# Kernel optimization log

Hardware: AMD Instinct MI355X
Metric: run time of the kernel (lower is better)

Reference implementation:

```python
import jax, jax.numpy as jnp
import numpy as np

B, N, D, H = 4, 2048, 256, 4
DH = D // H
SS = DH ** -0.25  # sqrt(scale), applied to both qk0 and qk1
EPS = 1e-5


def _split_heads(t):
    # [B, N, D] -> [B, H, N, DH]
    b, n, _ = t.shape
    return t.reshape(b, n, H, DH).transpose(0, 2, 1, 3)


def _merge_heads(t):
    # [B, H, N, DH] -> [B, N, D]
    b, h, n, dh = t.shape
    return t.transpose(0, 2, 1, 3).reshape(b, n, h * dh)


def _layernorm(x, g, b):
    mu = jnp.mean(x, axis=-1, keepdims=True)
    var = jnp.mean(jnp.square(x - mu), axis=-1, keepdims=True)
    return (x - mu) * jax.lax.rsqrt(var + EPS) * g + b


def setup_inputs() -> dict:
    key = jax.random.key(0)
    ks = jax.random.split(key, 16)
    s = 0.02
    return {
        "x0": jax.random.normal(ks[0], (B, N, D), jnp.float32),
        "x1": jax.random.normal(ks[1], (B, N, D), jnp.float32),
        # weights stored as [in, out] (y = x @ W + b), matching torch Linear math
        "Wqk": jax.random.normal(ks[2], (D, D), jnp.float32) * s,
        "bqk": jnp.zeros((D,), jnp.float32),
        "Wv": jax.random.normal(ks[3], (D, D), jnp.float32) * s,
        "bv": jnp.zeros((D,), jnp.float32),
        "Wo": jax.random.normal(ks[4], (D, D), jnp.float32) * s,
        "bo": jnp.zeros((D,), jnp.float32),
        "W1": jax.random.normal(ks[5], (2 * D, 2 * D), jnp.float32) * s,
        "b1": jnp.zeros((2 * D,), jnp.float32),
        "ln_g": jnp.ones((2 * D,), jnp.float32),
        "ln_b": jnp.zeros((2 * D,), jnp.float32),
        "W2": jax.random.normal(ks[6], (2 * D, D), jnp.float32) * s,
        "b2": jnp.zeros((D,), jnp.float32),
    }


def reference(x0, x1, Wqk, bqk, Wv, bv, Wo, bo, W1, b1, ln_g, ln_b, W2, b2):
    qk0 = _split_heads(x0 @ Wqk + bqk) * SS  # [B,H,N,DH]
    qk1 = _split_heads(x1 @ Wqk + bqk) * SS
    v0 = _split_heads(x0 @ Wv + bv)
    v1 = _split_heads(x1 @ Wv + bv)

    # single shared similarity matrix, reused for both softmax directions
    sim = jnp.einsum("bhid,bhjd->bhij", qk0, qk1)  # [B,H,N0,N1]
    attn01 = jax.nn.softmax(sim, axis=-1)                      # rows over j
    attn10 = jax.nn.softmax(jnp.swapaxes(sim, -1, -2), axis=-1)  # rows over i

    m0 = jnp.einsum("bhij,bhjd->bhid", attn01, v1)  # [B,H,N0,DH]
    m1 = jnp.einsum("bhji,bhjd->bhid", jnp.swapaxes(attn10, -1, -2), v0)

    m0 = _merge_heads(m0) @ Wo + bo  # [B,N,D]
    m1 = _merge_heads(m1) @ Wo + bo

    def ffn(x, m):
        h = jnp.concatenate([x, m], axis=-1) @ W1 + b1
        h = jax.nn.gelu(_layernorm(h, ln_g, ln_b), approximate=False)
        return x + h @ W2 + b2

    return ffn(x0, m0), ffn(x1, m1)
```

## Files before the change

### kernel.cpp

```cpp
#include <hip/hip_runtime.h>
#include <hip/hip_bf16.h>
#include <math.h>

#define DEV static __device__ __forceinline__

typedef float f32x4 __attribute__((ext_vector_type(4)));
typedef short s16x8 __attribute__((ext_vector_type(8)));
typedef unsigned short u16;
typedef unsigned int u32;
typedef u32 u32x2 __attribute__((ext_vector_type(2)));
typedef u16 u16x4 __attribute__((ext_vector_type(4)));

#define ROWS 16384
#define SSCALE 0.35355339059327379f

DEV f32x4 mfma16(s16x8 a, s16x8 b, f32x4 c) {
  return __builtin_amdgcn_mfma_f32_16x16x32_bf16(a, b, c, 0, 0, 0);
}

DEV float bf2f(u16 x) { u32 u = ((u32)x) << 16; float f; __builtin_memcpy(&f, &u, 4); return f; }
DEV u16 f2bf(float x) { __hip_bfloat16 b = __float2bfloat16(x); u16 r; __builtin_memcpy(&r, &b, 2); return r; }

DEV void gload_lds16(const void* g, void* l) {
  __builtin_amdgcn_global_load_lds((const __attribute__((address_space(1))) u32*)g,
                                   (__attribute__((address_space(3))) u32*)l, 16, 0, 0);
}

__global__ __launch_bounds__(256) void k_prep(
    const float* __restrict__ x0, const float* __restrict__ x1,
    const float* __restrict__ Wqk, const float* __restrict__ Wv,
    const float* __restrict__ Wo, const float* __restrict__ W1,
    const float* __restrict__ W2,
    u16* __restrict__ bt_qkv, u16* __restrict__ bt_o,
    u16* __restrict__ bt_1, u16* __restrict__ bt_2, u16* __restrict__ Xb)
{
  int tid = blockIdx.x * 256 + threadIdx.x;
  if (tid < 131072) {
    int c = tid >> 8, k = tid & 255;
    float v = (c < 256) ? Wqk[k * 256 + c] : Wv[k * 256 + (c - 256)];
    bt_qkv[tid] = f2bf(v);
  } else if (tid < 131072 + 65536) {
    int t = tid - 131072; int c = t >> 8, k = t & 255;
    bt_o[t] = f2bf(Wo[k * 256 + c]);
  } else if (tid < 131072 + 65536 + 262144) {
    int t = tid - (131072 + 65536); int c = t >> 9, k = t & 511;
    bt_1[t] = f2bf(W1[k * 512 + c]);
  } else if (tid < 589824) {
    int t = tid - (131072 + 65536 + 262144); int c = t >> 9, k = t & 511;
    bt_2[t] = f2bf(W2[k * 256 + c]);
  } else {
    int t = tid - 589824;
    float v = (t < 8192 * 256) ? x0[t] : x1[t - 8192 * 256];
    Xb[t] = f2bf(v);
  }
}

template <int KD, int K1, int EPI, int BN>
__global__ __launch_bounds__(256, 2) void k_gemm(
    const u16* __restrict__ A1, const u16* __restrict__ A2,
    const u16* __restrict__ Bt,
    const float* __restrict__ bias, const float* __restrict__ bias2,
    const float* __restrict__ res0, const float* __restrict__ res1,
    u16* __restrict__ outb, u16* __restrict__ outb2,
    float* __restrict__ outf, int Ncols)
{
  constexpr int MR = (BN == 128) ? 4 : 2;
  __shared__ char lds[16384 + 2 * BN * 64];
  char* ldsA = lds;
  char* ldsB = lds + 16384;
  const int tid = threadIdx.x;
  const int lane = tid & 63;
  const int w = tid >> 6;
  const int wm = (BN == 128) ? (w >> 1) : w;
  const int wn = (BN == 128) ? (w & 1) : 0;
  const int g = lane >> 4, li = lane & 15;
  const int m0 = blockIdx.x * 128, n0 = blockIdx.y * BN;

  auto stage = [&](int buf, int t) {
    const int k0 = t * 32;
#pragma unroll
    for (int it = 0; it < 2; ++it) {
      int chunk = it * 256 + w * 64 + lane;
      int row = chunk >> 2, c = chunk & 3;
      int kc = k0 + ((c ^ ((row >> 1) & 3)) << 3);
      const u16* src = (kc < K1) ? (A1 + (size_t)(m0 + row) * K1 + kc)
                                 : (A2 + (size_t)(m0 + row) * (KD - K1) + (kc - K1));
      gload_lds16(src, ldsA + buf * 8192 + (it * 256 + w * 64) * 16);
    }
#pragma unroll
    for (int it = 0; it < BN / 64; ++it) {
      int chunk = it * 256 + w * 64 + lane;
      int row = chunk >> 2, c = chunk & 3;
      int kc = k0 + ((c ^ ((row >> 1) & 3)) << 3);
      gload_lds16(Bt + (size_t)(n0 + row) * KD + kc,
                  ldsB + buf * (BN * 64) + (it * 256 + w * 64) * 16);
    }
  };

  f32x4 acc[MR][4] = {};

  stage(0, 0);
  __syncthreads();
  const int NT = KD / 32;
  for (int t = 0; t < NT; ++t) {
    if (t + 1 < NT) stage((t + 1) & 1, t + 1);
    const char* bufA = ldsA + (t & 1) * 8192;
    const char* bufB = ldsB + (t & 1) * (BN * 64);
    s16x8 af[MR], bfr[4];
#pragma unroll
    for (int rt = 0; rt < MR; ++rt) {
      int row = wm * (MR * 16) + rt * 16 + li;
      af[rt] = *(const s16x8*)(bufA + row * 64 + ((g ^ ((row >> 1) & 3)) << 4));
    }
#pragma unroll
    for (int ct = 0; ct < 4; ++ct) {
      int col = wn * 64 + ct * 16 + li;
      bfr[ct] = *(const s16x8*)(bufB + col * 64 + ((g ^ ((col >> 1) & 3)) << 4));
    }
#pragma unroll
    for (int rt = 0; rt < MR; ++rt)
#pragma unroll
      for (int ct = 0; ct < 4; ++ct)
        acc[rt][ct] = mfma16(af[rt], bfr[ct], acc[rt][ct]);
    __syncthreads();
  }

#pragma unroll
  for (int rt = 0; rt < MR; ++rt) {
#pragma unroll
    for (int ct = 0; ct < 4; ++ct) {
      const int growb = m0 + wm * (MR * 16) + rt * 16 + g * 4;
      const int gcol = n0 + wn * 64 + ct * 16 + li;
      if (EPI == 0) {
        const int dir = growb >> 13, b = (growb >> 11) & 3, n = growb & 2047;
        if (gcol < 256) {
          const int h = gcol >> 6, dh = gcol & 63;
#pragma unroll
          for (int r = 0; r < 4; ++r) {
            float q = (acc[rt][ct][r] + bias[gcol]) * SSCALE;
            outb[((size_t)(dir * 16 + b * 4 + h) * 2048 + (n + r)) * 64 + dh] = f2bf(q);
          }
        } else {
          const int c2 = gcol - 256, h = c2 >> 6, dh = c2 & 63;
          u16x4 pk;
#pragma unroll
          for (int r = 0; r < 4; ++r) pk[r] = f2bf(acc[rt][ct][r] + bias2[c2]);
          *(u16x4*)(outb2 + ((size_t)(dir * 16 + b * 4 + h) * 64 + dh) * 2048 + n) = pk;
        }
      } else if (EPI == 1) {
#pragma unroll
        for (int r = 0; r < 4; ++r)
          outb[(size_t)(growb + r) * Ncols + gcol] = f2bf(acc[rt][ct][r] + bias[gcol]);
      } else {
#pragma unroll
        for (int r = 0; r < 4; ++r) {
          int grow = growb + r;
          float x = (grow < 8192) ? res0[(size_t)grow * 256 + gcol]
                                  : res1[(size_t)(grow - 8192) * 256 + gcol];
          outf[(size_t)grow * 256 + gcol] = acc[rt][ct][r] + bias[gcol] + x;
        }
      }
    }
  }
}

__global__ __launch_bounds__(256, 3) void k_attn(
    const u16* __restrict__ qk, const u16* __restrict__ vt,
    float* __restrict__ Opart, float* __restrict__ lpart)
{
  __shared__ char Kl[2][8192];
  __shared__ char Vl[2][8192];
  __shared__ char Pl[4][4096];
  const int tid = threadIdx.x, lane = tid & 63, w = tid >> 6;
  const int g = lane >> 4, li = lane & 15;
  const int qblk = blockIdx.x & 15;
  const int half = (blockIdx.x >> 4) & 1;
  const int p = blockIdx.x >> 5;
  const int dir = p & 1;
  const int bh = p >> 1;
  const int pidx = dir * 16 + bh;
  const char* Qg = (const char*)qk + (size_t)pidx * 2048 * 128;
  const char* Kg = (const char*)qk + (size_t)((dir ^ 1) * 16 + bh) * 2048 * 128;
  const char* Vg = (const char*)vt + (size_t)((dir ^ 1) * 16 + bh) * 2048 * 128;
  const int q0 = qblk * 128 + w * 32;

  s16x8 qf[2][2];
#pragma unroll
  for (int qt = 0; qt < 2; ++qt)
#pragma unroll
    for (int ks = 0; ks < 2; ++ks)
      qf[qt][ks] = *(const s16x8*)(Qg + (size_t)(q0 + qt * 16 + li) * 128 + ks * 64 + g * 16);

  auto stageKV = [&](int buf, int jt) {
    const size_t krow0 = (size_t)(half * 1024 + jt * 64);
#pragma unroll
    for (int it = 0; it < 2; ++it) {
      int chunk = it * 256 + w * 64 + lane;
      int row = chunk >> 3, c = chunk & 7;
      int cc = (c ^ (row & 7)) << 4;
      gload_lds16(Kg + (krow0 + row) * 128 + cc, &Kl[buf][(it * 256 + w * 64) * 16]);
    }
#pragma unroll
    for (int it = 0; it < 2; ++it) {
      int chunk = it * 256 + w * 64 + lane;
      int row = chunk >> 3, c = chunk & 7;
      int cc = (c ^ (row & 7)) << 4;
      gload_lds16(Vg + (size_t)row * 4096 + half * 2048 + jt * 128 + cc,
                  &Vl[buf][(it * 256 + w * 64) * 16]);
    }
  };

  f32x4 acco[2][4] = {};
  float accl[2] = {0.f, 0.f};

  stageKV(0, 0);
  __syncthreads();
  for (int jt = 0; jt < 16; ++jt) {
    if (jt + 1 < 16) stageKV((jt + 1) & 1, jt + 1);
    const char* Kb = Kl[jt & 1];
    const char* Vb = Vl[jt & 1];

#pragma unroll
    for (int kt = 0; kt < 4; ++kt) {
      const int krow = kt * 16 + li;
      s16x8 kf0 = *(const s16x8*)(Kb + krow * 128 + ((g ^ (krow & 7)) << 4));
      s16x8 kf1 = *(const s16x8*)(Kb + krow * 128 + (((4 + g) ^ (krow & 7)) << 4));
#pragma unroll
      for (int qt = 0; qt < 2; ++qt) {
        f32x4 s = {0.f, 0.f, 0.f, 0.f};
        s = mfma16(kf0, qf[qt][0], s);
        s = mfma16(kf1, qf[qt][1], s);
        float p0 = __expf(s[0]), p1 = __expf(s[1]);
        float p2 = __expf(s[2]), p3 = __expf(s[3]);
        accl[qt] += (p0 + p1) + (p2 + p3);
        u32x2 pk;
        pk.x = (u32)f2bf(p0) | ((u32)f2bf(p1) << 16);
        pk.y = (u32)f2bf(p2) | ((u32)f2bf(p3) << 16);
        int addr = ((qt * 16 + li) * 128 + kt * 32 + g * 8) ^ ((li & 7) << 4);
        *(u32x2*)(&Pl[w][addr]) = pk;
      }
    }

#pragma unroll
    for (int ks = 0; ks < 2; ++ks) {
      s16x8 vfr[4];
#pragma unroll
      for (int dt = 0; dt < 4; ++dt) {
        const int vrow = dt * 16 + li;
        vfr[dt] = *(const s16x8*)(Vb + vrow * 128 + (((ks * 4 + g) ^ (vrow & 7)) << 4));
      }
#pragma unroll
      for (int qt = 0; qt < 2; ++qt) {
        s16x8 pf = *(const s16x8*)(
            &Pl[w][((qt * 16 + li) * 128 + ks * 64 + g * 16) ^ ((li & 7) << 4)]);
#pragma unroll
        for (int dt = 0; dt < 4; ++dt)
          acco[qt][dt] = mfma16(pf, vfr[dt], acco[qt][dt]);
      }
    }
    __syncthreads();
  }

#pragma unroll
  for (int qt = 0; qt < 2; ++qt) {
    float v = accl[qt];
    v += __shfl_xor(v, 16);
    v += __shfl_xor(v, 32);
    accl[qt] = v;
  }

  const int b = bh >> 2, h = bh & 3;
  const size_t rowbase = (size_t)dir * 8192 + (size_t)b * 2048 + q0;
  float* Oh = Opart + (size_t)half * 4194304;
#pragma unroll
  for (int qt = 0; qt < 2; ++qt)
#pragma unroll
    for (int dt = 0; dt < 4; ++dt)
#pragma unroll
      for (int r = 0; r < 4; ++r)
        Oh[(rowbase + qt * 16 + g * 4 + r) * 256 + h * 64 + dt * 16 + li] = acco[qt][dt][r];
  if (lane < 16) {
#pragma unroll
    for (int qt = 0; qt < 2; ++qt)
      lpart[half * 65536 + pidx * 2048 + q0 + qt * 16 + li] = accl[qt];
  }
}

__global__ __launch_bounds__(256) void k_combine(
    const float* __restrict__ Op, const float* __restrict__ lp,
    u16* __restrict__ m_all)
{
  int t = blockIdx.x * 256 + threadIdx.x;
  int row = t >> 6, quad = t & 63;
  int dh0 = quad * 4;
  int dir = row >> 13, b = (row >> 11) & 3, n = row & 2047, h = dh0 >> 6;
  int pidx = dir * 16 + b * 4 + h;
  float l = lp[pidx * 2048 + n] + lp[65536 + pidx * 2048 + n];
  float invl = 1.0f / l;
  f32x4 o0 = *(const f32x4*)(Op + (size_t)row * 256 + dh0);
  f32x4 o1 = *(const f32x4*)(Op + 4194304 + (size_t)row * 256 + dh0);
  u16x4 r4;
#pragma unroll
  for (int j = 0; j < 4; ++j) r4[j] = f2bf((o0[j] + o1[j]) * invl);
  *(u16x4*)(m_all + (size_t)row * 256 + dh0) = r4;
}

__global__ __launch_bounds__(256) void k_ln_gelu(
    const u16* __restrict__ h, const float* __restrict__ lg,
    const float* __restrict__ lb, u16* __restrict__ o)
{
  int lane = threadIdx.x & 63;
  size_t row = blockIdx.x * 4 + (threadIdx.x >> 6);
  s16x8 v = *(const s16x8*)(h + row * 512 + lane * 8);
  float f[8], s = 0.f, s2 = 0.f;
#pragma unroll
  for (int j = 0; j < 8; ++j) { f[j] = bf2f((u16)v[j]); s += f[j]; s2 += f[j] * f[j]; }
#pragma unroll
  for (int m = 1; m < 64; m <<= 1) { s += __shfl_xor(s, m); s2 += __shfl_xor(s2, m); }
  float mu = s * (1.0f / 512.0f);
  float var = s2 * (1.0f / 512.0f) - mu * mu;
  float rs = rsqrtf(var + 1e-5f);
  s16x8 ov;
#pragma unroll
  for (int j = 0; j < 8; ++j) {
    int c = lane * 8 + j;
    float y = (f[j] - mu) * rs * lg[c] + lb[c];
    float ge = 0.5f * y * (1.0f + erff(y * 0.70710678118654752f));
    ov[j] = (short)f2bf(ge);
  }
  *(s16x8*)(o + row * 512 + lane * 8) = ov;
}

extern "C" void kernel_launch(void* const* d_in, const int* in_sizes, int n_in,
                              void* d_out, int out_size, void* d_ws, size_t ws_size,
                              hipStream_t stream)
{
  const float* x0  = (const float*)d_in[0];
  const float* x1  = (const float*)d_in[1];
  const float* Wqk = (const float*)d_in[2];
  const float* bqk = (const float*)d_in[3];
  const float* Wv  = (const float*)d_in[4];
  const float* bv  = (const float*)d_in[5];
  const float* Wo  = (const float*)d_in[6];
  const float* bo  = (const float*)d_in[7];
  const float* W1  = (const float*)d_in[8];
  const float* b1  = (const float*)d_in[9];
  const float* lg  = (const float*)d_in[10];
  const float* lb  = (const float*)d_in[11];
  const float* W2  = (const float*)d_in[12];
  const float* b2  = (const float*)d_in[13];
  float* out = (float*)d_out;
  char* ws = (char*)d_ws;

  u16*   Xb    = (u16*)(ws + 0);
  u16*   qk    = (u16*)(ws + 8388608);
  u16*   vt    = (u16*)(ws + 16777216);
  u16*   m_all = (u16*)(ws + 25165824);
  float* lpart = (float*)(ws + 33554432);
  u16*   mo    = (u16*)(ws + 34078720);
  float* Opart = (float*)(ws + 42467328);
  u16*   hpre  = (u16*)(ws + 42467328);
  u16*   gact  = (u16*)(ws + 59244544);
  u16*   btqkv = (u16*)(ws + 76021760);
  u16*   bto   = (u16*)(ws + 76283904);
  u16*   bt1   = (u16*)(ws + 76414976);
  u16*   bt2   = (u16*)(ws + 76939264);

  k_prep<<<dim3(18688), dim3(256), 0, stream>>>(x0, x1, Wqk, Wv, Wo, W1, W2,
                                                btqkv, bto, bt1, bt2, Xb);
  k_gemm<256, 256, 0, 128><<<dim3(128, 4), dim3(256), 0, stream>>>(
      Xb, nullptr, btqkv, bqk, bv, nullptr, nullptr, qk, vt, nullptr, 512);
  k_attn<<<dim3(1024), dim3(256), 0, stream>>>(qk, vt, Opart, lpart);
  k_combine<<<dim3(4096), dim3(256), 0, stream>>>(Opart, lpart, m_all);
  k_gemm<256, 256, 1, 64><<<dim3(128, 4), dim3(256), 0, stream>>>(
      m_all, nullptr, bto, bo, nullptr, nullptr, nullptr, mo, nullptr, nullptr, 256);
  k_gemm<512, 256, 1, 128><<<dim3(128, 4), dim3(256), 0, stream>>>(
      Xb, mo, bt1, b1, nullptr, nullptr, nullptr, hpre, nullptr, nullptr, 512);
  k_ln_gelu<<<dim3(4096), dim3(256), 0, stream>>>(hpre, lg, lb, gact);
  k_gemm<512, 512, 3, 64><<<dim3(128, 4), dim3(256), 0, stream>>>(
      gact, nullptr, bt2, b2, nullptr, x0, x1, nullptr, nullptr, out, 256);
}
```

Before: 235.7 us.

## Fold Wo into W1, drop split-KV attention and combine, vectorize prep

Folds the output projection algebraically into the first FFN weight: computes Wo·W1[256:] and a folded bias in the prep kernel, which removes the Wo GEMM and its intermediate buffer. The attention kernel no longer splits KV into halves. Each block now processes 64 query rows over all 2048 keys and normalizes in-kernel, so the fp32 partial outputs and the combine kernel go away. Prep is rewritten with vectorized conversion and LDS-tiled weight transposes, and the attention grid uses a swizzled block order. The trade-offs are a serial 256-length dot product per folded weight element in prep, less per-block Q reuse in attention, and an extra bf16 rounding of the folded weights.

```diff
diff --git a/kernel.cpp b/kernel.cpp
--- a/kernel.cpp
+++ b/kernel.cpp
@@ -10,8 +10,8 @@
 typedef unsigned int u32;
 typedef u32 u32x2 __attribute__((ext_vector_type(2)));
 typedef u16 u16x4 __attribute__((ext_vector_type(4)));
-
-#define ROWS 16384
+typedef u16 u16x8 __attribute__((ext_vector_type(8)));
+
 #define SSCALE 0.35355339059327379f
 
 DEV f32x4 mfma16(s16x8 a, s16x8 b, f32x4 c) {
@@ -30,28 +30,67 @@
     const float* __restrict__ x0, const float* __restrict__ x1,
     const float* __restrict__ Wqk, const float* __restrict__ Wv,
     const float* __restrict__ Wo, const float* __restrict__ W1,
-    const float* __restrict__ W2,
-    u16* __restrict__ bt_qkv, u16* __restrict__ bt_o,
-    u16* __restrict__ bt_1, u16* __restrict__ bt_2, u16* __restrict__ Xb)
-{
-  int tid = blockIdx.x * 256 + threadIdx.x;
-  if (tid < 131072) {
-    int c = tid >> 8, k = tid & 255;
-    float v = (c < 256) ? Wqk[k * 256 + c] : Wv[k * 256 + (c - 256)];
-    bt_qkv[tid] = f2bf(v);
-  } else if (tid < 131072 + 65536) {
-    int t = tid - 131072; int c = t >> 8, k = t & 255;
-    bt_o[t] = f2bf(Wo[k * 256 + c]);
-  } else if (tid < 131072 + 65536 + 262144) {
-    int t = tid - (131072 + 65536); int c = t >> 9, k = t & 511;
-    bt_1[t] = f2bf(W1[k * 512 + c]);
-  } else if (tid < 589824) {
-    int t = tid - (131072 + 65536 + 262144); int c = t >> 9, k = t & 511;
-    bt_2[t] = f2bf(W2[k * 256 + c]);
+    const float* __restrict__ W2, const float* __restrict__ bo,
+    const float* __restrict__ b1,
+    u16* __restrict__ btqkv, u16* __restrict__ btF,
+    u16* __restrict__ bt2, float* __restrict__ bc, u16* __restrict__ Xb)
+{
+  const int blk = blockIdx.x, tid = threadIdx.x;
+  if (blk < 2048) {
+    int idx = blk * 2048 + tid * 8;
+    const float* src = (idx < 2097152) ? (x0 + idx) : (x1 + (idx - 2097152));
+    f32x4 va = *(const f32x4*)src;
+    f32x4 vb = *(const f32x4*)(src + 4);
+    u16x8 o;
+#pragma unroll
+    for (int j = 0; j < 4; ++j) { o[j] = f2bf(va[j]); o[4 + j] = f2bf(vb[j]); }
+    *(u16x8*)(Xb + idx) = o;
+  } else if (blk < 2144) {
+    __shared__ float T[64][65];
+    int tb = blk - 2048;
+    const float* src; u16* dst; int sld, dld, kr0, c0, drow0;
+    if (tb < 16)      { src = Wqk; dst = btqkv; sld = 256; dld = 256; drow0 = 0;
+                        kr0 = (tb >> 2) * 64; c0 = (tb & 3) * 64; }
+    else if (tb < 32) { tb -= 16; src = Wv; dst = btqkv; sld = 256; dld = 256; drow0 = 256;
+                        kr0 = (tb >> 2) * 64; c0 = (tb & 3) * 64; }
+    else if (tb < 64) { tb -= 32; src = W1; dst = btF; sld = 512; dld = 512; drow0 = 0;
+                        kr0 = (tb >> 3) * 64; c0 = (tb & 7) * 64; }
+    else              { tb -= 64; src = W2; dst = bt2; sld = 256; dld = 512; drow0 = 0;
+                        kr0 = (tb >> 2) * 64; c0 = (tb & 3) * 64; }
+    int r = tid >> 2, cq = (tid & 3) * 16;
+#pragma unroll
+    for (int q = 0; q < 4; ++q) {
+      f32x4 v = *(const f32x4*)(src + (size_t)(kr0 + r) * sld + c0 + cq + q * 4);
+#pragma unroll
+      for (int e = 0; e < 4; ++e) T[r][cq + q * 4 + e] = v[e];
+    }
+    __syncthreads();
+    int c = tid >> 2, kq = (tid & 3) * 16;
+#pragma unroll
+    for (int q = 0; q < 2; ++q) {
+      u16x8 o;
+#pragma unroll
+      for (int e = 0; e < 8; ++e) o[e] = f2bf(T[kq + q * 8 + e][c]);
+      *(u16x8*)(dst + (size_t)(drow0 + c0 + c) * dld + kr0 + kq + q * 8) = o;
+    }
+  } else if (blk < 2656) {
+    int wb = blk - 2144;
+    int i = wb >> 1;
+    int n = (wb & 1) * 256 + tid;
+    float a0 = 0.f, a1 = 0.f, a2 = 0.f, a3 = 0.f;
+    for (int j = 0; j < 256; j += 4) {
+      a0 = fmaf(Wo[i * 256 + j],     W1[(size_t)(256 + j) * 512 + n], a0);
+      a1 = fmaf(Wo[i * 256 + j + 1], W1[(size_t)(257 + j) * 512 + n], a1);
+      a2 = fmaf(Wo[i * 256 + j + 2], W1[(size_t)(258 + j) * 512 + n], a2);
+      a3 = fmaf(Wo[i * 256 + j + 3], W1[(size_t)(259 + j) * 512 + n], a3);
+    }
+    btF[(size_t)n * 512 + 256 + i] = f2bf((a0 + a1) + (a2 + a3));
   } else {
-    int t = tid - 589824;
-    float v = (t < 8192 * 256) ? x0[t] : x1[t - 8192 * 256];
-    Xb[t] = f2bf(v);
+    int n = (blk - 2656) * 256 + tid;
+    float acc = b1[n];
+    for (int j = 0; j < 256; ++j)
+      acc = fmaf(bo[j], W1[(size_t)(256 + j) * 512 + n], acc);
+    bc[n] = acc;
   }
 }
 
@@ -132,20 +171,20 @@
       const int growb = m0 + wm * (MR * 16) + rt * 16 + g * 4;
       const int gcol = n0 + wn * 64 + ct * 16 + li;
       if (EPI == 0) {
-        const int dir = growb >> 13, b = (growb >> 11) & 3, n = growb & 2047;
+        const int dir = growb >> 13, bb = (growb >> 11) & 3, n = growb & 2047;
         if (gcol < 256) {
           const int h = gcol >> 6, dh = gcol & 63;
 #pragma unroll
           for (int r = 0; r < 4; ++r) {
             float q = (acc[rt][ct][r] + bias[gcol]) * SSCALE;
-            outb[((size_t)(dir * 16 + b * 4 + h) * 2048 + (n + r)) * 64 + dh] = f2bf(q);
+            outb[((size_t)(dir * 16 + bb * 4 + h) * 2048 + (n + r)) * 64 + dh] = f2bf(q);
           }
         } else {
           const int c2 = gcol - 256, h = c2 >> 6, dh = c2 & 63;
           u16x4 pk;
 #pragma unroll
           for (int r = 0; r < 4; ++r) pk[r] = f2bf(acc[rt][ct][r] + bias2[c2]);
-          *(u16x4*)(outb2 + ((size_t)(dir * 16 + b * 4 + h) * 64 + dh) * 2048 + n) = pk;
+          *(u16x4*)(outb2 + ((size_t)(dir * 16 + bb * 4 + h) * 64 + dh) * 2048 + n) = pk;
         }
       } else if (EPI == 1) {
 #pragma unroll
@@ -164,145 +203,97 @@
   }
 }
 
-__global__ __launch_bounds__(256, 3) void k_attn(
-    const u16* __restrict__ qk, const u16* __restrict__ vt,
-    float* __restrict__ Opart, float* __restrict__ lpart)
+__global__ __launch_bounds__(256, 4) void k_attn(
+    const u16* __restrict__ qk, const u16* __restrict__ vt, u16* __restrict__ m_all)
 {
   __shared__ char Kl[2][8192];
   __shared__ char Vl[2][8192];
-  __shared__ char Pl[4][4096];
+  __shared__ char Pl[4][2048];
   const int tid = threadIdx.x, lane = tid & 63, w = tid >> 6;
   const int g = lane >> 4, li = lane & 15;
-  const int qblk = blockIdx.x & 15;
-  const int half = (blockIdx.x >> 4) & 1;
-  const int p = blockIdx.x >> 5;
-  const int dir = p & 1;
-  const int bh = p >> 1;
-  const int pidx = dir * 16 + bh;
-  const char* Qg = (const char*)qk + (size_t)pidx * 2048 * 128;
-  const char* Kg = (const char*)qk + (size_t)((dir ^ 1) * 16 + bh) * 2048 * 128;
-  const char* Vg = (const char*)vt + (size_t)((dir ^ 1) * 16 + bh) * 2048 * 128;
-  const int q0 = qblk * 128 + w * 32;
-
-  s16x8 qf[2][2];
-#pragma unroll
-  for (int qt = 0; qt < 2; ++qt)
-#pragma unroll
-    for (int ks = 0; ks < 2; ++ks)
-      qf[qt][ks] = *(const s16x8*)(Qg + (size_t)(q0 + qt * 16 + li) * 128 + ks * 64 + g * 16);
+  const int sw = (blockIdx.x & 7) * 128 + (blockIdx.x >> 3);
+  const int qblk = sw & 31;
+  const int p = sw >> 5;
+  const int dir = p >> 4, bh = p & 15;
+  const char* Qg = (const char*)qk + (size_t)p * 262144;
+  const char* Kg = (const char*)qk + (size_t)((dir ^ 1) * 16 + bh) * 262144;
+  const char* Vg = (const char*)vt + (size_t)((dir ^ 1) * 16 + bh) * 262144;
+  const int q0 = qblk * 64 + w * 16;
+
+  s16x8 qf0 = *(const s16x8*)(Qg + (size_t)(q0 + li) * 128 + g * 16);
+  s16x8 qf1 = *(const s16x8*)(Qg + (size_t)(q0 + li) * 128 + 64 + g * 16);
 
   auto stageKV = [&](int buf, int jt) {
-    const size_t krow0 = (size_t)(half * 1024 + jt * 64);
 #pragma unroll
     for (int it = 0; it < 2; ++it) {
       int chunk = it * 256 + w * 64 + lane;
       int row = chunk >> 3, c = chunk & 7;
       int cc = (c ^ (row & 7)) << 4;
-      gload_lds16(Kg + (krow0 + row) * 128 + cc, &Kl[buf][(it * 256 + w * 64) * 16]);
+      gload_lds16(Kg + (size_t)(jt * 64 + row) * 128 + cc, &Kl[buf][(it * 256 + w * 64) * 16]);
     }
 #pragma unroll
     for (int it = 0; it < 2; ++it) {
       int chunk = it * 256 + w * 64 + lane;
       int row = chunk >> 3, c = chunk & 7;
       int cc = (c ^ (row & 7)) << 4;
-      gload_lds16(Vg + (size_t)row * 4096 + half * 2048 + jt * 128 + cc,
-                  &Vl[buf][(it * 256 + w * 64) * 16]);
+      gload_lds16(Vg + (size_t)row * 4096 + jt * 128 + cc, &Vl[buf][(it * 256 + w * 64) * 16]);
     }
   };
 
-  f32x4 acco[2][4] = {};
-  float accl[2] = {0.f, 0.f};
+  f32x4 acco[4] = {};
+  float accl = 0.f;
 
   stageKV(0, 0);
   __syncthreads();
-  for (int jt = 0; jt < 16; ++jt) {
-    if (jt + 1 < 16) stageKV((jt + 1) & 1, jt + 1);
+  for (int jt = 0; jt < 32; ++jt) {
+    if (jt + 1 < 32) stageKV((jt + 1) & 1, jt + 1);
     const char* Kb = Kl[jt & 1];
     const char* Vb = Vl[jt & 1];
 
 #pragma unroll
     for (int kt = 0; kt < 4; ++kt) {
       const int krow = kt * 16 + li;
-      s16x8 kf0 = *(const s16x8*)(Kb + krow * 128 + ((g ^ (krow & 7)) << 4));
-      s16x8 kf1 = *(const s16x8*)(Kb + krow * 128 + (((4 + g) ^ (krow & 7)) << 4));
-#pragma unroll
-      for (int qt = 0; qt < 2; ++qt) {
-        f32x4 s = {0.f, 0.f, 0.f, 0.f};
-        s = mfma16(kf0, qf[qt][0], s);
-        s = mfma16(kf1, qf[qt][1], s);
-        float p0 = __expf(s[0]), p1 = __expf(s[1]);
-        float p2 = __expf(s[2]), p3 = __expf(s[3]);
-        accl[qt] += (p0 + p1) + (p2 + p3);
-        u32x2 pk;
-        pk.x = (u32)f2bf(p0) | ((u32)f2bf(p1) << 16);
-        pk.y = (u32)f2bf(p2) | ((u32)f2bf(p3) << 16);
-        int addr = ((qt * 16 + li) * 128 + kt * 32 + g * 8) ^ ((li & 7) << 4);
-        *(u32x2*)(&Pl[w][addr]) = pk;
-      }
+      s16x8 kf0 = *(const s16x8*)(Kb + krow * 128 + ((g ^ (li & 7)) << 4));
+      s16x8 kf1 = *(const s16x8*)(Kb + krow * 128 + (((4 + g) ^ (li & 7)) << 4));
+      f32x4 s = {0.f, 0.f, 0.f, 0.f};
+      s = mfma16(kf0, qf0, s);
+      s = mfma16(kf1, qf1, s);
+      float p0 = __expf(s[0]), p1 = __expf(s[1]);
+      float p2 = __expf(s[2]), p3 = __expf(s[3]);
+      accl += (p0 + p1) + (p2 + p3);
+      u32x2 pk;
+      pk.x = (u32)f2bf(p0) | ((u32)f2bf(p1) << 16);
+      pk.y = (u32)f2bf(p2) | ((u32)f2bf(p3) << 16);
+      *(u32x2*)(&Pl[w][(li * 128 + kt * 32 + g * 8) ^ ((li & 7) << 4)]) = pk;
     }
 
 #pragma unroll
     for (int ks = 0; ks < 2; ++ks) {
-      s16x8 vfr[4];
+      s16x8 pf = *(const s16x8*)(&Pl[w][(li * 128 + ks * 64 + g * 16) ^ ((li & 7) << 4)]);
 #pragma unroll
       for (int dt = 0; dt < 4; ++dt) {
         const int vrow = dt * 16 + li;
-        vfr[dt] = *(const s16x8*)(Vb + vrow * 128 + (((ks * 4 + g) ^ (vrow & 7)) << 4));
+        s16x8 vfr = *(const s16x8*)(Vb + vrow * 128 + (((ks * 4 + g) ^ (li & 7)) << 4));
+        acco[dt] = mfma16(pf, vfr, acco[dt]);
       }
-#pragma unroll
-      for (int qt = 0; qt < 2; ++qt) {
-        s16x8 pf = *(const s16x8*)(
-            &Pl[w][((qt * 16 + li) * 128 + ks * 64 + g * 16) ^ ((li & 7) << 4)]);
-#pragma unroll
-        for (int dt = 0; dt < 4; ++dt)
-          acco[qt][dt] = mfma16(pf, vfr[dt], acco[qt][dt]);
-      }
     }
     __syncthreads();
   }
 
-#pragma unroll
-  for (int qt = 0; qt < 2; ++qt) {
-    float v = accl[qt];
-    v += __shfl_xor(v, 16);
-    v += __shfl_xor(v, 32);
-    accl[qt] = v;
-  }
-
-  const int b = bh >> 2, h = bh & 3;
-  const size_t rowbase = (size_t)dir * 8192 + (size_t)b * 2048 + q0;
-  float* Oh = Opart + (size_t)half * 4194304;
-#pragma unroll
-  for (int qt = 0; qt < 2; ++qt)
-#pragma unroll
-    for (int dt = 0; dt < 4; ++dt)
-#pragma unroll
-      for (int r = 0; r < 4; ++r)
-        Oh[(rowbase + qt * 16 + g * 4 + r) * 256 + h * 64 + dt * 16 + li] = acco[qt][dt][r];
-  if (lane < 16) {
-#pragma unroll
-    for (int qt = 0; qt < 2; ++qt)
-      lpart[half * 65536 + pidx * 2048 + q0 + qt * 16 + li] = accl[qt];
-  }
-}
-
-__global__ __launch_bounds__(256) void k_combine(
-    const float* __restrict__ Op, const float* __restrict__ lp,
-    u16* __restrict__ m_all)
-{
-  int t = blockIdx.x * 256 + threadIdx.x;
-  int row = t >> 6, quad = t & 63;
-  int dh0 = quad * 4;
-  int dir = row >> 13, b = (row >> 11) & 3, n = row & 2047, h = dh0 >> 6;
-  int pidx = dir * 16 + b * 4 + h;
-  float l = lp[pidx * 2048 + n] + lp[65536 + pidx * 2048 + n];
-  float invl = 1.0f / l;
-  f32x4 o0 = *(const f32x4*)(Op + (size_t)row * 256 + dh0);
-  f32x4 o1 = *(const f32x4*)(Op + 4194304 + (size_t)row * 256 + dh0);
-  u16x4 r4;
-#pragma unroll
-  for (int j = 0; j < 4; ++j) r4[j] = f2bf((o0[j] + o1[j]) * invl);
-  *(u16x4*)(m_all + (size_t)row * 256 + dh0) = r4;
+  accl += __shfl_xor(accl, 16);
+  accl += __shfl_xor(accl, 32);
+  float inv = 1.0f / accl;
+  float invq[4];
+#pragma unroll
+  for (int r = 0; r < 4; ++r) invq[r] = __shfl(inv, g * 4 + r);
+
+  const int bb = bh >> 2, h = bh & 3;
+  const size_t rowb = (size_t)dir * 8192 + (size_t)bb * 2048 + q0 + g * 4;
+#pragma unroll
+  for (int dt = 0; dt < 4; ++dt)
+#pragma unroll
+    for (int r = 0; r < 4; ++r)
+      m_all[(rowb + r) * 256 + h * 64 + dt * 16 + li] = f2bf(acco[dt][r] * invq[r]);
 }
 
 __global__ __launch_bounds__(256) void k_ln_gelu(
@@ -356,26 +347,20 @@
   u16*   qk    = (u16*)(ws + 8388608);
   u16*   vt    = (u16*)(ws + 16777216);
   u16*   m_all = (u16*)(ws + 25165824);
-  float* lpart = (float*)(ws + 33554432);
-  u16*   mo    = (u16*)(ws + 34078720);
-  float* Opart = (float*)(ws + 42467328);
-  u16*   hpre  = (u16*)(ws + 42467328);
-  u16*   gact  = (u16*)(ws + 59244544);
-  u16*   btqkv = (u16*)(ws + 76021760);
-  u16*   bto   = (u16*)(ws + 76283904);
-  u16*   bt1   = (u16*)(ws + 76414976);
-  u16*   bt2   = (u16*)(ws + 76939264);
-
-  k_prep<<<dim3(18688), dim3(256), 0, stream>>>(x0, x1, Wqk, Wv, Wo, W1, W2,
-                                                btqkv, bto, bt1, bt2, Xb);
+  u16*   hpre  = (u16*)(ws + 33554432);
+  u16*   gact  = (u16*)(ws + 50331648);
+  u16*   btqkv = (u16*)(ws + 67108864);
+  u16*   btF   = (u16*)(ws + 67371008);
+  u16*   bt2   = (u16*)(ws + 67895296);
+  float* bc    = (float*)(ws + 68419584);
+
+  k_prep<<<dim3(2658), dim3(256), 0, stream>>>(x0, x1, Wqk, Wv, Wo, W1, W2, bo, b1,
+                                               btqkv, btF, bt2, bc, Xb);
   k_gemm<256, 256, 0, 128><<<dim3(128, 4), dim3(256), 0, stream>>>(
       Xb, nullptr, btqkv, bqk, bv, nullptr, nullptr, qk, vt, nullptr, 512);
-  k_attn<<<dim3(1024), dim3(256), 0, stream>>>(qk, vt, Opart, lpart);
-  k_combine<<<dim3(4096), dim3(256), 0, stream>>>(Opart, lpart, m_all);
-  k_gemm<256, 256, 1, 64><<<dim3(128, 4), dim3(256), 0, stream>>>(
-      m_all, nullptr, bto, bo, nullptr, nullptr, nullptr, mo, nullptr, nullptr, 256);
+  k_attn<<<dim3(1024), dim3(256), 0, stream>>>(qk, vt, m_all);
   k_gemm<512, 256, 1, 128><<<dim3(128, 4), dim3(256), 0, stream>>>(
-      Xb, mo, bt1, b1, nullptr, nullptr, nullptr, hpre, nullptr, nullptr, 512);
+      Xb, m_all, btF, bc, nullptr, nullptr, nullptr, hpre, nullptr, nullptr, 512);
   k_ln_gelu<<<dim3(4096), dim3(256), 0, stream>>>(hpre, lg, lb, gact);
   k_gemm<512, 512, 3, 64><<<dim3(128, 4), dim3(256), 0, stream>>>(
       gact, nullptr, bt2, b2, nullptr, x0, x1, nullptr, nullptr, out, 256);
```

Result: no change. 238.1 us (+1.0%).
